# Performance work log

Measured on AMD Instinct MI355X. Metric: run time of the kernel, lower is better.

Reference implementation:

```python
import jax, jax.numpy as jnp
import numpy as np

N_CLASSES = 256
PER_CLASS = 128
N_SUPPORT = 5
N_QUERY = PER_CLASS - N_SUPPORT  # 123
N_VIEW = 2
D = 384
N = N_CLASSES * PER_CLASS  # 32768


def setup_inputs() -> dict:
    key = jax.random.key(0)
    k1, k2 = jax.random.split(key, 2)
    reps = jax.random.normal(k1, (N, N_VIEW, D), dtype=jnp.float32)
    # block-sorted labels: class c occupies rows [c*PER_CLASS, (c+1)*PER_CLASS)
    labels = (jnp.arange(N, dtype=jnp.int32) // PER_CLASS).astype(jnp.int32)
    return {"reps": reps, "labels": labels}


def reference(reps, labels):
    # labels are block-sorted per class, so the original's
    # labels.eq(c).nonzero()[:n_support] / [n_support:] gathers are static reshapes.
    reps_r = reps.reshape(N_CLASSES, PER_CLASS, N_VIEW, D)
    # class-mean prototypes over the support set: [C, V, D]
    prototypes = reps_r[:, :N_SUPPORT].mean(axis=1)
    # query samples: [C*N_QUERY, V, D]
    queries = reps_r[:, N_SUPPORT:].reshape(N_CLASSES * N_QUERY, N_VIEW, D)

    x2 = jnp.sum(queries * queries, axis=-1)            # [n, V]
    y2 = jnp.sum(prototypes * prototypes, axis=-1)      # [m, V]
    xy = jnp.einsum('nvd,mvd->nmv', queries, prototypes)  # [n, m, V]
    dists = x2[:, None, :] + y2[None, :, :] - 2.0 * xy

    # log_softmax over the prototype (class) axis
    log_p_y = jax.nn.log_softmax(-dists, axis=1)
    log_p_y = log_p_y.reshape(N_CLASSES, N_QUERY, N_CLASSES, N_VIEW)

    # gather the true-class log-prob for each query / view
    cls = jnp.arange(N_CLASSES)
    correct = log_p_y[cls, :, cls, :]  # [C, N_QUERY, V]
    loss = -correct.mean()
    return loss
```

## Files before the change

### kernel.cpp

```cpp
#include <hip/hip_runtime.h>
#include <hip/hip_bf16.h>
#include <math.h>

#define NCLS 256
#define PER_CLASS 128
#define NSUP 5
#define NQRY 123
#define NVIEW 2
#define DD 384
#define NQ_TOT (NCLS * NQRY)
#define BM 128
#define BK 32
#define NKT (DD / BK)
#define QS 40
#define PS 32

typedef __attribute__((ext_vector_type(8))) short short8;
typedef __attribute__((ext_vector_type(4))) float floatx4;

union FragU { uint4 u; short8 s; };
union PkU { __hip_bfloat162 b2; unsigned int u; };

__device__ __forceinline__ unsigned int cvt2bf(float lo, float hi) {
    PkU p;
    p.b2 = __float22bfloat162_rn(make_float2(lo, hi));
    return p.u;
}

__device__ __forceinline__ void gll16(const ushort* g, ushort* l) {
    __builtin_amdgcn_global_load_lds(
        (const __attribute__((address_space(1))) unsigned int*)g,
        (__attribute__((address_space(3))) unsigned int*)l, 16, 0, 0);
}

#define BARRIER() asm volatile("s_waitcnt lgkmcnt(0)\n\ts_barrier" ::: "memory")
#define WAITVM(n) asm volatile("s_waitcnt vmcnt(" #n ")" ::: "memory")

__global__ __launch_bounds__(384) void proto_kernel(const float* __restrict__ reps,
                                                    ushort* __restrict__ pbf,
                                                    float* __restrict__ y2,
                                                    float* __restrict__ out) {
    __shared__ float wp[6];
    const int b = blockIdx.x;
    const int c = b & 255, v = b >> 8;
    const int d = threadIdx.x;
    if (b == 0 && d == 0) out[0] = 0.f;
    const float* p = reps + ((size_t)(c * PER_CLASS) * NVIEW + v) * DD + d;
    float s = 0.f;
#pragma unroll
    for (int k = 0; k < NSUP; ++k) s += p[(size_t)k * NVIEW * DD];
    s *= 0.2f;
    __hip_bfloat16 h = __float2bfloat16(s);
    pbf[(size_t)b * DD + d] = *reinterpret_cast<ushort*>(&h);
    float q = s * s;
#pragma unroll
    for (int o = 1; o < 64; o <<= 1) q += __shfl_xor(q, o);
    if ((d & 63) == 0) wp[d >> 6] = q;
    __syncthreads();
    if (d == 0) y2[b] = wp[0] + wp[1] + wp[2] + wp[3] + wp[4] + wp[5];
}

__global__ __launch_bounds__(256, 2) void main_kernel(const float* __restrict__ reps,
                                                      const ushort* __restrict__ pbf,
                                                      const float* __restrict__ y2g,
                                                      float* __restrict__ out) {
    __shared__ ushort q_lds[2][BM * QS];
    __shared__ ushort p_lds[2][NCLS * PS];
    __shared__ float pmx[BM][2];
    __shared__ float pse[BM][2];
    __shared__ float wred[8];

    const int t = threadIdx.x;
    const int v = blockIdx.y;
    const int q0 = blockIdx.x * BM;
    const int wave = t >> 6;
    const int lane = t & 63;
    const int col = lane & 15;
    const int quad = lane >> 4;
    const int wm = wave >> 1;
    const int wn = wave & 1;

    const int sq = t >> 1;
    const int h16 = (t & 1) * 16;
    const int nq = q0 + sq;
    const float* qsrc = reps +
        (size_t)((nq / NQRY) * PER_CLASS + NSUP + (nq % NQRY)) * (NVIEW * DD) + v * DD + h16;

    const ushort* psrc = pbf + (size_t)(v * NCLS + wave * 64 + (lane >> 2)) * DD
                             + (((lane & 3) ^ ((lane >> 3) & 3)) << 3);

    const int sP = (col >> 1) & 3;
    int boff[8];
#pragma unroll
    for (int nt = 0; nt < 8; ++nt)
        boff[nt] = (wn * 128 + nt * 16 + col) * PS + ((quad ^ sP) << 3);

    floatx4 acc[4][8];
#pragma unroll
    for (int mt = 0; mt < 4; ++mt)
#pragma unroll
        for (int nt = 0; nt < 8; ++nt) acc[mt][nt] = (floatx4)0.f;

    float4 qfA[4], qfB[4];

#define LOADQ(kt, R)                                                               \
    do {                                                                           \
        _Pragma("unroll") for (int i = 0; i < 4; ++i)                              \
            R[i] = *(const float4*)(qsrc + (kt) * BK + i * 4);                     \
    } while (0)

#define GLLP(kt, b)                                                                \
    do {                                                                           \
        _Pragma("unroll") for (int i = 0; i < 4; ++i)                              \
            gll16(psrc + i * (16 * DD) + (kt) * BK,                                \
                  &p_lds[b][wave * 2048 + i * 512]);                               \
    } while (0)

#define STAGEQ(b, R)                                                               \
    do {                                                                           \
        uint4 w0, w1;                                                              \
        w0.x = cvt2bf(R[0].x, R[0].y); w0.y = cvt2bf(R[0].z, R[0].w);              \
        w0.z = cvt2bf(R[1].x, R[1].y); w0.w = cvt2bf(R[1].z, R[1].w);              \
        w1.x = cvt2bf(R[2].x, R[2].y); w1.y = cvt2bf(R[2].z, R[2].w);              \
        w1.z = cvt2bf(R[3].x, R[3].y); w1.w = cvt2bf(R[3].z, R[3].w);              \
        *(uint4*)&q_lds[b][sq * QS + h16] = w0;                                    \
        *(uint4*)&q_lds[b][sq * QS + h16 + 8] = w1;                                \
    } while (0)

#define COMPUTE(b)                                                                 \
    do {                                                                           \
        short8 af[4];                                                              \
        _Pragma("unroll") for (int mt = 0; mt < 4; ++mt) {                         \
            FragU f;                                                               \
            f.u = *(const uint4*)&q_lds[b][(wm * 64 + mt * 16 + col) * QS + quad * 8]; \
            af[mt] = f.s;                                                          \
        }                                                                          \
        _Pragma("unroll") for (int nt = 0; nt < 8; ++nt) {                         \
            FragU bb;                                                              \
            bb.u = *(const uint4*)&p_lds[b][boff[nt]];                             \
            _Pragma("unroll") for (int mt = 0; mt < 4; ++mt)                       \
                acc[mt][nt] = __builtin_amdgcn_mfma_f32_16x16x32_bf16(af[mt], bb.s, acc[mt][nt], 0, 0, 0); \
        }                                                                          \
    } while (0)

    LOADQ(0, qfA); GLLP(0, 0);
    LOADQ(1, qfB); GLLP(1, 1);
    WAITVM(8);
    STAGEQ(0, qfA);
    BARRIER();

#pragma unroll
    for (int kt = 0; kt < NKT; ++kt) {
        COMPUTE(kt & 1);
        if (kt == NKT - 1) break;
        BARRIER();
        if (kt + 2 < NKT) {
            if ((kt & 1) == 0) { LOADQ(kt + 2, qfA); } else { LOADQ(kt + 2, qfB); }
            GLLP(kt + 2, kt & 1);
            WAITVM(8);
        } else {
            WAITVM(0);
        }
        if ((kt & 1) == 0) STAGEQ(1, qfB); else STAGEQ(0, qfA);
        BARRIER();
    }

    float y2c[8];
#pragma unroll
    for (int nt = 0; nt < 8; ++nt) y2c[nt] = y2g[v * NCLS + wn * 128 + nt * 16 + col];

    float corr = 0.f;
#pragma unroll
    for (int mt = 0; mt < 4; ++mt) {
#pragma unroll
        for (int r = 0; r < 4; ++r) {
            const int qloc = wm * 64 + mt * 16 + quad * 4 + r;
            const int n = q0 + qloc;
            const int cn = n / NQRY;
            float s[8];
            float mx = -1e30f;
#pragma unroll
            for (int nt = 0; nt < 8; ++nt) {
                s[nt] = 2.f * acc[mt][nt][r] - y2c[nt];
                mx = fmaxf(mx, s[nt]);
                if (cn == wn * 128 + nt * 16 + col) corr += s[nt];
            }
#pragma unroll
            for (int o = 1; o < 16; o <<= 1) mx = fmaxf(mx, __shfl_xor(mx, o));
            float e = 0.f;
#pragma unroll
            for (int nt = 0; nt < 8; ++nt) e += __expf(s[nt] - mx);
#pragma unroll
            for (int o = 1; o < 16; o <<= 1) e += __shfl_xor(e, o);
            if (col == 0) { pmx[qloc][wn] = mx; pse[qloc][wn] = e; }
        }
    }
#pragma unroll
    for (int o = 1; o < 64; o <<= 1) corr += __shfl_xor(corr, o);
    if (lane == 0) wred[wave] = corr;
    __syncthreads();

    float lval = 0.f;
    if (t < BM) {
        float m0 = pmx[t][0], m1 = pmx[t][1];
        float M = fmaxf(m0, m1);
        float E = pse[t][0] * __expf(m0 - M) + pse[t][1] * __expf(m1 - M);
        lval = M + __logf(E);
    }
#pragma unroll
    for (int o = 1; o < 64; o <<= 1) lval += __shfl_xor(lval, o);
    if (lane == 0) wred[4 + wave] = lval;
    __syncthreads();

    if (t == 0) {
        float tot = (wred[4] + wred[5] + wred[6] + wred[7]) -
                    (wred[0] + wred[1] + wred[2] + wred[3]);
        atomicAdd(out, tot * (1.f / (float)(NQ_TOT * NVIEW)));
    }
}

extern "C" void kernel_launch(void* const* d_in, const int* in_sizes, int n_in,
                              void* d_out, int out_size, void* d_ws, size_t ws_size,
                              hipStream_t stream) {
    const float* reps = (const float*)d_in[0];
    float* ws = (float*)d_ws;
    ushort* pbf = (ushort*)ws;
    float* y2 = (float*)(pbf + NVIEW * NCLS * DD);
    float* out = (float*)d_out;

    proto_kernel<<<dim3(NVIEW * NCLS), dim3(DD), 0, stream>>>(reps, pbf, y2, out);
    main_kernel<<<dim3(NQ_TOT / BM, NVIEW), dim3(256), 0, stream>>>(reps, pbf, y2, out);
}
```

Measured before the change: 162.4 us.

## Load query fragments directly to registers and triple-buffer prototype tiles

Query rows are no longer staged through LDS. Each lane loads its own fp32 slice of the query straight from global memory in MFMA fragment layout and converts it to bf16 in registers. Prototype tiles move to a three-buffer LDS ring, which cuts the loop to one barrier per k-step and drops the LDS write and read traffic for queries. In exchange, query loads are issued in the same iteration that consumes them, so their global latency is no longer hidden behind earlier work. The two waves that share a row block also now read the same query data twice from global memory.

```diff
diff --git a/kernel.cpp b/kernel.cpp
--- a/kernel.cpp
+++ b/kernel.cpp
@@ -12,8 +12,8 @@
 #define BM 128
 #define BK 32
 #define NKT (DD / BK)
-#define QS 40
 #define PS 32
+#define NBUF 3
 
 typedef __attribute__((ext_vector_type(8))) short short8;
 typedef __attribute__((ext_vector_type(4))) float floatx4;
@@ -64,8 +64,7 @@
                                                       const ushort* __restrict__ pbf,
                                                       const float* __restrict__ y2g,
                                                       float* __restrict__ out) {
-    __shared__ ushort q_lds[2][BM * QS];
-    __shared__ ushort p_lds[2][NCLS * PS];
+    __shared__ ushort p_lds[NBUF][NCLS * PS];
     __shared__ float pmx[BM][2];
     __shared__ float pse[BM][2];
     __shared__ float wred[8];
@@ -80,20 +79,20 @@
     const int wm = wave >> 1;
     const int wn = wave & 1;
 
-    const int sq = t >> 1;
-    const int h16 = (t & 1) * 16;
-    const int nq = q0 + sq;
-    const float* qsrc = reps +
-        (size_t)((nq / NQRY) * PER_CLASS + NSUP + (nq % NQRY)) * (NVIEW * DD) + v * DD + h16;
-
     const ushort* psrc = pbf + (size_t)(v * NCLS + wave * 64 + (lane >> 2)) * DD
                              + (((lane & 3) ^ ((lane >> 3) & 3)) << 3);
 
     const int sP = (col >> 1) & 3;
-    int boff[8];
-#pragma unroll
-    for (int nt = 0; nt < 8; ++nt)
-        boff[nt] = (wn * 128 + nt * 16 + col) * PS + ((quad ^ sP) << 3);
+    const int pbase = (wn * 128 + col) * PS + ((quad ^ sP) << 3);
+
+    const float* qb[4];
+#pragma unroll
+    for (int mt = 0; mt < 4; ++mt) {
+        const int nq = q0 + wm * 64 + mt * 16 + col;
+        qb[mt] = reps +
+            (size_t)((nq / NQRY) * PER_CLASS + NSUP + (nq % NQRY)) * (NVIEW * DD) +
+            v * DD + quad * 8;
+    }
 
     floatx4 acc[4][8];
 #pragma unroll
@@ -101,12 +100,14 @@
 #pragma unroll
         for (int nt = 0; nt < 8; ++nt) acc[mt][nt] = (floatx4)0.f;
 
-    float4 qfA[4], qfB[4];
-
-#define LOADQ(kt, R)                                                               \
+    float4 qv[4][2];
+
+#define LOADQ(kt)                                                                  \
     do {                                                                           \
-        _Pragma("unroll") for (int i = 0; i < 4; ++i)                              \
-            R[i] = *(const float4*)(qsrc + (kt) * BK + i * 4);                     \
+        _Pragma("unroll") for (int mt = 0; mt < 4; ++mt) {                         \
+            qv[mt][0] = *(const float4*)(qb[mt] + (kt) * BK);                      \
+            qv[mt][1] = *(const float4*)(qb[mt] + (kt) * BK + 4);                  \
+        }                                                                          \
     } while (0)
 
 #define GLLP(kt, b)                                                                \
@@ -116,53 +117,41 @@
                   &p_lds[b][wave * 2048 + i * 512]);                               \
     } while (0)
 
-#define STAGEQ(b, R)                                                               \
-    do {                                                                           \
-        uint4 w0, w1;                                                              \
-        w0.x = cvt2bf(R[0].x, R[0].y); w0.y = cvt2bf(R[0].z, R[0].w);              \
-        w0.z = cvt2bf(R[1].x, R[1].y); w0.w = cvt2bf(R[1].z, R[1].w);              \
-        w1.x = cvt2bf(R[2].x, R[2].y); w1.y = cvt2bf(R[2].z, R[2].w);              \
-        w1.z = cvt2bf(R[3].x, R[3].y); w1.w = cvt2bf(R[3].z, R[3].w);              \
-        *(uint4*)&q_lds[b][sq * QS + h16] = w0;                                    \
-        *(uint4*)&q_lds[b][sq * QS + h16 + 8] = w1;                                \
-    } while (0)
-
 #define COMPUTE(b)                                                                 \
     do {                                                                           \
         short8 af[4];                                                              \
         _Pragma("unroll") for (int mt = 0; mt < 4; ++mt) {                         \
             FragU f;                                                               \
-            f.u = *(const uint4*)&q_lds[b][(wm * 64 + mt * 16 + col) * QS + quad * 8]; \
+            f.u.x = cvt2bf(qv[mt][0].x, qv[mt][0].y);                              \
+            f.u.y = cvt2bf(qv[mt][0].z, qv[mt][0].w);                              \
+            f.u.z = cvt2bf(qv[mt][1].x, qv[mt][1].y);                              \
+            f.u.w = cvt2bf(qv[mt][1].z, qv[mt][1].w);                              \
             af[mt] = f.s;                                                          \
         }                                                                          \
         _Pragma("unroll") for (int nt = 0; nt < 8; ++nt) {                         \
             FragU bb;                                                              \
-            bb.u = *(const uint4*)&p_lds[b][boff[nt]];                             \
+            bb.u = *(const uint4*)&p_lds[b][pbase + nt * 16 * PS];                 \
             _Pragma("unroll") for (int mt = 0; mt < 4; ++mt)                       \
                 acc[mt][nt] = __builtin_amdgcn_mfma_f32_16x16x32_bf16(af[mt], bb.s, acc[mt][nt], 0, 0, 0); \
         }                                                                          \
     } while (0)
 
-    LOADQ(0, qfA); GLLP(0, 0);
-    LOADQ(1, qfB); GLLP(1, 1);
-    WAITVM(8);
-    STAGEQ(0, qfA);
+    GLLP(0, 0);
+    GLLP(1, 1);
+    WAITVM(4);
     BARRIER();
 
 #pragma unroll
     for (int kt = 0; kt < NKT; ++kt) {
-        COMPUTE(kt & 1);
-        if (kt == NKT - 1) break;
-        BARRIER();
-        if (kt + 2 < NKT) {
-            if ((kt & 1) == 0) { LOADQ(kt + 2, qfA); } else { LOADQ(kt + 2, qfB); }
-            GLLP(kt + 2, kt & 1);
-            WAITVM(8);
+        if (kt < NKT - 2) GLLP(kt + 2, (kt + 2) % NBUF);
+        LOADQ(kt);
+        if (kt < NKT - 2) {
+            WAITVM(12);
         } else {
             WAITVM(0);
         }
-        if ((kt & 1) == 0) STAGEQ(1, qfB); else STAGEQ(0, qfA);
-        BARRIER();
+        COMPUTE(kt % NBUF);
+        if (kt < NKT - 1) BARRIER();
     }
 
     float y2c[8];
```

Measured after the change: 174.3 us. 7.3% more time.

## Use 512-thread blocks with 2x4 wave grid and reuse LDS for epilogue

Applied to the files above, without the earlier changes.

Doubles the threads per block to 8 waves arranged 2x4 over the 128-query by 256-class tile, so each wave holds a 64x64 accumulator instead of 64x128. This cuts accumulator registers per thread so more waves can be resident, which should hide memory latency better. Query and prototype loads are split across more threads. The softmax partial reductions now reuse the prototype LDS buffer instead of separate shared arrays. The cost is more A-fragment LDS reads relative to MFMA work and wider cross-wave reductions.

```diff
diff --git a/kernel.cpp b/kernel.cpp
--- a/kernel.cpp
+++ b/kernel.cpp
@@ -60,15 +60,12 @@
     if (d == 0) y2[b] = wp[0] + wp[1] + wp[2] + wp[3] + wp[4] + wp[5];
 }
 
-__global__ __launch_bounds__(256, 2) void main_kernel(const float* __restrict__ reps,
+__global__ __launch_bounds__(512, 4) void main_kernel(const float* __restrict__ reps,
                                                       const ushort* __restrict__ pbf,
                                                       const float* __restrict__ y2g,
                                                       float* __restrict__ out) {
     __shared__ ushort q_lds[2][BM * QS];
     __shared__ ushort p_lds[2][NCLS * PS];
-    __shared__ float pmx[BM][2];
-    __shared__ float pse[BM][2];
-    __shared__ float wred[8];
 
     const int t = threadIdx.x;
     const int v = blockIdx.y;
@@ -77,54 +74,47 @@
     const int lane = t & 63;
     const int col = lane & 15;
     const int quad = lane >> 4;
-    const int wm = wave >> 1;
-    const int wn = wave & 1;
-
-    const int sq = t >> 1;
-    const int h16 = (t & 1) * 16;
+    const int wm = wave >> 2;
+    const int wn = wave & 3;
+
+    const int sq = t >> 2;
+    const int f8 = (t & 3) * 8;
     const int nq = q0 + sq;
     const float* qsrc = reps +
-        (size_t)((nq / NQRY) * PER_CLASS + NSUP + (nq % NQRY)) * (NVIEW * DD) + v * DD + h16;
-
-    const ushort* psrc = pbf + (size_t)(v * NCLS + wave * 64 + (lane >> 2)) * DD
+        (size_t)((nq / NQRY) * PER_CLASS + NSUP + (nq % NQRY)) * (NVIEW * DD) + v * DD + f8;
+
+    const ushort* psrc = pbf + (size_t)(v * NCLS + wave * 32 + (lane >> 2)) * DD
                              + (((lane & 3) ^ ((lane >> 3) & 3)) << 3);
 
     const int sP = (col >> 1) & 3;
-    int boff[8];
-#pragma unroll
-    for (int nt = 0; nt < 8; ++nt)
-        boff[nt] = (wn * 128 + nt * 16 + col) * PS + ((quad ^ sP) << 3);
-
-    floatx4 acc[4][8];
+    const int pbase = (wn * 64 + col) * PS + ((quad ^ sP) << 3);
+
+    floatx4 acc[4][4];
 #pragma unroll
     for (int mt = 0; mt < 4; ++mt)
 #pragma unroll
-        for (int nt = 0; nt < 8; ++nt) acc[mt][nt] = (floatx4)0.f;
-
-    float4 qfA[4], qfB[4];
+        for (int nt = 0; nt < 4; ++nt) acc[mt][nt] = (floatx4)0.f;
+
+    float4 qfA[2], qfB[2];
 
 #define LOADQ(kt, R)                                                               \
     do {                                                                           \
-        _Pragma("unroll") for (int i = 0; i < 4; ++i)                              \
-            R[i] = *(const float4*)(qsrc + (kt) * BK + i * 4);                     \
+        R[0] = *(const float4*)(qsrc + (kt) * BK);                                 \
+        R[1] = *(const float4*)(qsrc + (kt) * BK + 4);                             \
     } while (0)
 
 #define GLLP(kt, b)                                                                \
     do {                                                                           \
-        _Pragma("unroll") for (int i = 0; i < 4; ++i)                              \
-            gll16(psrc + i * (16 * DD) + (kt) * BK,                                \
-                  &p_lds[b][wave * 2048 + i * 512]);                               \
+        gll16(psrc + (kt) * BK, &p_lds[b][wave * 1024]);                           \
+        gll16(psrc + 16 * DD + (kt) * BK, &p_lds[b][wave * 1024 + 512]);           \
     } while (0)
 
 #define STAGEQ(b, R)                                                               \
     do {                                                                           \
-        uint4 w0, w1;                                                              \
-        w0.x = cvt2bf(R[0].x, R[0].y); w0.y = cvt2bf(R[0].z, R[0].w);              \
-        w0.z = cvt2bf(R[1].x, R[1].y); w0.w = cvt2bf(R[1].z, R[1].w);              \
-        w1.x = cvt2bf(R[2].x, R[2].y); w1.y = cvt2bf(R[2].z, R[2].w);              \
-        w1.z = cvt2bf(R[3].x, R[3].y); w1.w = cvt2bf(R[3].z, R[3].w);              \
-        *(uint4*)&q_lds[b][sq * QS + h16] = w0;                                    \
-        *(uint4*)&q_lds[b][sq * QS + h16 + 8] = w1;                                \
+        uint4 w;                                                                   \
+        w.x = cvt2bf(R[0].x, R[0].y); w.y = cvt2bf(R[0].z, R[0].w);                \
+        w.z = cvt2bf(R[1].x, R[1].y); w.w = cvt2bf(R[1].z, R[1].w);                \
+        *(uint4*)&q_lds[b][sq * QS + f8] = w;                                      \
     } while (0)
 
 #define COMPUTE(b)                                                                 \
@@ -135,9 +125,9 @@
             f.u = *(const uint4*)&q_lds[b][(wm * 64 + mt * 16 + col) * QS + quad * 8]; \
             af[mt] = f.s;                                                          \
         }                                                                          \
-        _Pragma("unroll") for (int nt = 0; nt < 8; ++nt) {                         \
+        _Pragma("unroll") for (int nt = 0; nt < 4; ++nt) {                         \
             FragU bb;                                                              \
-            bb.u = *(const uint4*)&p_lds[b][boff[nt]];                             \
+            bb.u = *(const uint4*)&p_lds[b][pbase + nt * 16 * PS];                 \
             _Pragma("unroll") for (int mt = 0; mt < 4; ++mt)                       \
                 acc[mt][nt] = __builtin_amdgcn_mfma_f32_16x16x32_bf16(af[mt], bb.s, acc[mt][nt], 0, 0, 0); \
         }                                                                          \
@@ -145,7 +135,7 @@
 
     LOADQ(0, qfA); GLLP(0, 0);
     LOADQ(1, qfB); GLLP(1, 1);
-    WAITVM(8);
+    WAITVM(4);
     STAGEQ(0, qfA);
     BARRIER();
 
@@ -154,10 +144,10 @@
         COMPUTE(kt & 1);
         if (kt == NKT - 1) break;
         BARRIER();
-        if (kt + 2 < NKT) {
+        if (kt < NKT - 2) {
             if ((kt & 1) == 0) { LOADQ(kt + 2, qfA); } else { LOADQ(kt + 2, qfB); }
             GLLP(kt + 2, kt & 1);
-            WAITVM(8);
+            WAITVM(4);
         } else {
             WAITVM(0);
         }
@@ -165,9 +155,15 @@
         BARRIER();
     }
 
-    float y2c[8];
-#pragma unroll
-    for (int nt = 0; nt < 8; ++nt) y2c[nt] = y2g[v * NCLS + wn * 128 + nt * 16 + col];
+    __syncthreads();
+    float* eplds = (float*)&p_lds[0][0];
+    float (*pmx)[4] = (float(*)[4])eplds;
+    float (*pse)[4] = (float(*)[4])(eplds + 512);
+    float* wred = eplds + 1024;
+
+    float y2c[4];
+#pragma unroll
+    for (int nt = 0; nt < 4; ++nt) y2c[nt] = y2g[v * NCLS + wn * 64 + nt * 16 + col];
 
     float corr = 0.f;
 #pragma unroll
@@ -177,19 +173,19 @@
             const int qloc = wm * 64 + mt * 16 + quad * 4 + r;
             const int n = q0 + qloc;
             const int cn = n / NQRY;
-            float s[8];
+            float s[4];
             float mx = -1e30f;
 #pragma unroll
-            for (int nt = 0; nt < 8; ++nt) {
+            for (int nt = 0; nt < 4; ++nt) {
                 s[nt] = 2.f * acc[mt][nt][r] - y2c[nt];
                 mx = fmaxf(mx, s[nt]);
-                if (cn == wn * 128 + nt * 16 + col) corr += s[nt];
+                if (cn == wn * 64 + nt * 16 + col) corr += s[nt];
             }
 #pragma unroll
             for (int o = 1; o < 16; o <<= 1) mx = fmaxf(mx, __shfl_xor(mx, o));
             float e = 0.f;
 #pragma unroll
-            for (int nt = 0; nt < 8; ++nt) e += __expf(s[nt] - mx);
+            for (int nt = 0; nt < 4; ++nt) e += __expf(s[nt] - mx);
 #pragma unroll
             for (int o = 1; o < 16; o <<= 1) e += __shfl_xor(e, o);
             if (col == 0) { pmx[qloc][wn] = mx; pse[qloc][wn] = e; }
@@ -202,19 +198,22 @@
 
     float lval = 0.f;
     if (t < BM) {
-        float m0 = pmx[t][0], m1 = pmx[t][1];
-        float M = fmaxf(m0, m1);
-        float E = pse[t][0] * __expf(m0 - M) + pse[t][1] * __expf(m1 - M);
+        float m0 = pmx[t][0], m1 = pmx[t][1], m2 = pmx[t][2], m3 = pmx[t][3];
+        float M = fmaxf(fmaxf(m0, m1), fmaxf(m2, m3));
+        float E = pse[t][0] * __expf(m0 - M) + pse[t][1] * __expf(m1 - M) +
+                  pse[t][2] * __expf(m2 - M) + pse[t][3] * __expf(m3 - M);
         lval = M + __logf(E);
     }
 #pragma unroll
     for (int o = 1; o < 64; o <<= 1) lval += __shfl_xor(lval, o);
-    if (lane == 0) wred[4 + wave] = lval;
+    if (lane == 0) wred[8 + wave] = lval;
     __syncthreads();
 
     if (t == 0) {
-        float tot = (wred[4] + wred[5] + wred[6] + wred[7]) -
-                    (wred[0] + wred[1] + wred[2] + wred[3]);
+        float tot = (wred[8] + wred[9] + wred[10] + wred[11] +
+                     wred[12] + wred[13] + wred[14] + wred[15]) -
+                    (wred[0] + wred[1] + wred[2] + wred[3] +
+                     wred[4] + wred[5] + wred[6] + wred[7]);
         atomicAdd(out, tot * (1.f / (float)(NQ_TOT * NVIEW)));
     }
 }
@@ -229,5 +228,5 @@
     float* out = (float*)d_out;
 
     proto_kernel<<<dim3(NVIEW * NCLS), dim3(DD), 0, stream>>>(reps, pbf, y2, out);
-    main_kernel<<<dim3(NQ_TOT / BM, NVIEW), dim3(256), 0, stream>>>(reps, pbf, y2, out);
-}
+    main_kernel<<<dim3(NQ_TOT / BM, NVIEW), dim3(512), 0, stream>>>(reps, pbf, y2, out);
+}
```

New measurement: 165.5 us. No clear change (+2.0%).
